# Kernel tuning notes

Measured on AMD Instinct MI355X. Metric: run time of the kernel, lower is better.

## Reference

```python
import jax, jax.numpy as jnp
import numpy as np

D_MODEL = 2048
NUM_HEADS = 16
D_K = D_MODEL // NUM_HEADS  # 128
THETA = 10000.0
BATCH = 2
SEQ = 2048


def _rope(v, pos):
    # v: [..., S, d_k], pos: [..., S] int
    half = v.shape[-1] // 2
    inv_freq = THETA ** (-(jnp.arange(half, dtype=jnp.float32) * 2.0) / v.shape[-1])
    ang = pos[..., None].astype(jnp.float32) * inv_freq  # [..., S, half]
    cos, sin = jnp.cos(ang), jnp.sin(ang)
    x1 = v[..., 0::2]
    x2 = v[..., 1::2]
    r1 = x1 * cos - x2 * sin
    r2 = x1 * sin + x2 * cos
    return jnp.stack([r1, r2], axis=-1).reshape(v.shape)


def setup_inputs() -> dict:
    key = jax.random.key(0)
    ks = jax.random.split(key, 5)
    scale = D_MODEL ** -0.5
    x = jax.random.normal(ks[0], (BATCH, SEQ, D_MODEL), dtype=jnp.float32)
    WQ = jax.random.normal(ks[1], (D_MODEL, D_MODEL), dtype=jnp.float32) * scale
    WK = jax.random.normal(ks[2], (D_MODEL, D_MODEL), dtype=jnp.float32) * scale
    WV = jax.random.normal(ks[3], (D_MODEL, D_MODEL), dtype=jnp.float32) * scale
    WO = jax.random.normal(ks[4], (D_MODEL, D_MODEL), dtype=jnp.float32) * scale
    token_positions = jnp.broadcast_to(jnp.arange(SEQ, dtype=jnp.int32), (BATCH, SEQ))
    return {"x": x, "token_positions": token_positions, "WQ": WQ, "WK": WK, "WV": WV, "WO": WO}


def reference(x, token_positions, WQ, WK, WV, WO):
    B, S, _ = x.shape
    split = lambda t: t.reshape(B, S, NUM_HEADS, D_K).transpose(0, 2, 1, 3)  # [B,H,S,d]
    Q = split(x @ WQ.T)
    K = split(x @ WK.T)
    V = split(x @ WV.T)
    pos = token_positions[:, None, :]  # broadcast over heads
    Q = _rope(Q, pos)
    K = _rope(K, pos)
    scores = jnp.einsum('bhqd,bhkd->bhqk', Q, K) / np.sqrt(D_K).astype(np.float32)
    causal = jnp.arange(S)[:, None] >= jnp.arange(S)[None, :]  # [S,S]
    scores = jnp.where(causal, scores, -jnp.inf)
    attn = jax.nn.softmax(scores, axis=-1)
    out = jnp.einsum('bhqk,bhkd->bhqd', attn, V)
    out = out.transpose(0, 2, 1, 3).reshape(B, S, D_MODEL)
    return out @ WO.T
```

## Files before the change

### kernel.cpp

```cpp
#include <hip/hip_runtime.h>

typedef unsigned short ushort;
typedef __attribute__((ext_vector_type(8))) __bf16 bf16x8;
typedef __attribute__((ext_vector_type(8))) ushort ushort8;
typedef __attribute__((ext_vector_type(4))) float f32x4;
typedef __attribute__((ext_vector_type(16))) float f32x16;
typedef __attribute__((ext_vector_type(4))) unsigned u32x4;

#define DM 2048
#define NH 16
#define DK 128
#define BATCH 2
#define SEQ 2048
#define MROWS (BATCH*SEQ)

#define GLDS16(g, l) __builtin_amdgcn_global_load_lds(                         \
    (const __attribute__((address_space(1))) void*)(g),                        \
    (__attribute__((address_space(3))) void*)(l), 16, 0, 0)

__device__ __forceinline__ ushort f2bf(float f) {
  unsigned u = __builtin_bit_cast(unsigned, f);
  u += 0x7fffu + ((u >> 16) & 1u);
  return (ushort)(u >> 16);
}

__device__ __forceinline__ unsigned cvtpk(float lo, float hi) {
  unsigned r;
  asm("v_cvt_pk_bf16_f32 %0, %1, %2" : "=v"(r) : "v"(lo), "v"(hi));
  return r;
}

__global__ __launch_bounds__(256) void cvt_all(const float* __restrict__ x,
                                               const float* __restrict__ w0,
                                               const float* __restrict__ w1,
                                               const float* __restrict__ w2,
                                               const float* __restrict__ w3,
                                               ushort* __restrict__ xb,
                                               ushort* __restrict__ o0,
                                               ushort* __restrict__ o1,
                                               ushort* __restrict__ o2,
                                               ushort* __restrict__ o3) {
  int b = blockIdx.x;
  const float* src;
  ushort* dst;
  int lb;
  if (b < 4096) { src = x; dst = xb; lb = b; }
  else {
    int wsel = (b - 4096) >> 11;
    lb = (b - 4096) & 2047;
    src = (wsel == 0) ? w0 : (wsel == 1) ? w1 : (wsel == 2) ? w2 : w3;
    dst = (wsel == 0) ? o0 : (wsel == 1) ? o1 : (wsel == 2) ? o2 : o3;
  }
  int i = lb * 256 + threadIdx.x;
  const float4* p = (const float4*)src;
  float4 a = p[2 * i], bq = p[2 * i + 1];
  ushort8 o;
  o[0] = f2bf(a.x); o[1] = f2bf(a.y); o[2] = f2bf(a.z); o[3] = f2bf(a.w);
  o[4] = f2bf(bq.x); o[5] = f2bf(bq.y); o[6] = f2bf(bq.z); o[7] = f2bf(bq.w);
  *(ushort8*)(dst + (size_t)8 * i) = o;
}

template <int NW, int NFR, int MODE>
__device__ __forceinline__ void gemmF_body(const ushort* __restrict__ A,
                                           const ushort* __restrict__ B0,
                                           const ushort* __restrict__ B1,
                                           const ushort* __restrict__ B2,
                                           ushort* __restrict__ O0,
                                           ushort* __restrict__ O1,
                                           ushort* __restrict__ O2,
                                           float* __restrict__ ofp,
                                           int row0, int col0) {
  extern __shared__ ushort lds[];
  constexpr int NT = DM / 64;
  constexpr int BUFSZ = 8192 + NW * NFR * 4096;
  const ushort* Bw[3] = {B0, B1, B2};
  ushort* Ow[3] = {O0, O1, O2};
  const int tid = threadIdx.x;
  const int wid = tid >> 6, lane = tid & 63;
  const int l15 = lane & 15, lhi = lane >> 4;
  const int wm = wid >> 2, wn = wid & 3;
  const int swz = l15 & 7;

  f32x4 acc[4][NW * NFR];
  const f32x4 z4 = {0.f, 0.f, 0.f, 0.f};
#pragma unroll
  for (int mq = 0; mq < 4; ++mq)
#pragma unroll
    for (int i = 0; i < NW * NFR; ++i) acc[mq][i] = z4;

  auto stage = [&](int kt, int buf) {
    ushort* dstA = &lds[buf * BUFSZ];
    const ushort* srcA = A + (size_t)row0 * DM + kt * 64;
#pragma unroll
    for (int j = 0; j < 2; ++j) {
      int g = j * 512 + tid;
      int r = g >> 3, c = g & 7;
      GLDS16(srcA + (size_t)r * DM + ((c ^ (r & 7)) * 8),
             &dstA[(j * 512 + wid * 64) * 8]);
    }
#pragma unroll
    for (int w3 = 0; w3 < NW; ++w3) {
      ushort* dstB = &lds[buf * BUFSZ + 8192 + w3 * NFR * 4096];
      const ushort* srcB = Bw[w3] + (size_t)col0 * DM + kt * 64;
#pragma unroll
      for (int j = 0; j < NFR; ++j) {
        int g = j * 512 + tid;
        int r = g >> 3, c = g & 7;
        GLDS16(srcB + (size_t)r * DM + ((c ^ (r & 7)) * 8),
               &dstB[(j * 512 + wid * 64) * 8]);
      }
    }
  };

  stage(0, 0);
  asm volatile("s_waitcnt vmcnt(0)" ::: "memory");
  asm volatile("s_barrier" ::: "memory");

  for (int t = 0; t < NT; ++t) {
    const int cb = t & 1;
    const ushort* Ab = &lds[cb * BUFSZ];
    const ushort* Bb = Ab + 8192;
    if (t + 1 < NT) stage(t + 1, cb ^ 1);
#pragma unroll
    for (int ks = 0; ks < 2; ++ks) {
      bf16x8 af[4];
#pragma unroll
      for (int mq = 0; mq < 4; ++mq) {
        int row = wm * 64 + mq * 16 + l15;
        af[mq] = *(const bf16x8*)&Ab[row * 64 + (((ks * 4 + lhi) ^ swz) * 8)];
      }
      bf16x8 bfr[NW * NFR];
#pragma unroll
      for (int w3 = 0; w3 < NW; ++w3)
#pragma unroll
        for (int n = 0; n < NFR; ++n) {
          int row = wn * (NFR * 16) + n * 16 + l15;
          bfr[w3 * NFR + n] =
              *(const bf16x8*)&Bb[w3 * NFR * 4096 + row * 64 + (((ks * 4 + lhi) ^ swz) * 8)];
        }
      __builtin_amdgcn_s_setprio(1);
#pragma unroll
      for (int mq = 0; mq < 4; ++mq)
#pragma unroll
        for (int i = 0; i < NW * NFR; ++i)
          acc[mq][i] = __builtin_amdgcn_mfma_f32_16x16x32_bf16(af[mq], bfr[i], acc[mq][i], 0, 0, 0);
      __builtin_amdgcn_s_setprio(0);
    }
    asm volatile("s_waitcnt vmcnt(0)" ::: "memory");
    asm volatile("s_barrier" ::: "memory");
  }

#pragma unroll
  for (int mq = 0; mq < 4; ++mq) {
    int grow = row0 + wm * 64 + mq * 16 + lhi * 4;
#pragma unroll
    for (int w3 = 0; w3 < NW; ++w3)
#pragma unroll
      for (int n = 0; n < NFR; ++n) {
        int gcol = col0 + wn * (NFR * 16) + n * 16 + l15;
#pragma unroll
        for (int j = 0; j < 4; ++j) {
          float v = acc[mq][w3 * NFR + n][j];
          int r = grow + j;
          if (MODE == 0) {
            int b = r >> 11, s = r & (SEQ - 1);
            int h = gcol >> 7, d = gcol & (DK - 1);
            Ow[w3][((size_t)(b * NH + h) * SEQ + s) * DK + d] = f2bf(v);
          } else {
            ofp[(size_t)r * DM + gcol] = v;
          }
        }
      }
  }
}

__global__ __launch_bounds__(512, 2) void gemmF_qkv(const ushort* __restrict__ A,
                                                    const ushort* __restrict__ W0,
                                                    const ushort* __restrict__ W1,
                                                    const ushort* __restrict__ W2,
                                                    ushort* __restrict__ O0,
                                                    ushort* __restrict__ O1,
                                                    ushort* __restrict__ O2) {
  int f = ((int)blockIdx.x & 7) * 64 + ((int)blockIdx.x >> 3);
  int row0 = (f >> 4) * 128, col0 = (f & 15) * 128;
  gemmF_body<3, 2, 0>(A, W0, W1, W2, O0, O1, O2, nullptr, row0, col0);
}

__global__ __launch_bounds__(512, 2) void gemmF_out(const ushort* __restrict__ A,
                                                    const ushort* __restrict__ Bm,
                                                    float* __restrict__ ofp) {
  int f = ((int)blockIdx.x & 7) * 32 + ((int)blockIdx.x >> 3);
  int row0 = (f >> 3) * 128, col0 = (f & 7) * 256;
  gemmF_body<1, 4, 1>(A, Bm, nullptr, nullptr, nullptr, nullptr, nullptr, ofp, row0, col0);
}

__global__ __launch_bounds__(256) void rope_kernel(ushort* __restrict__ Q,
                                                   ushort* __restrict__ K,
                                                   const int* __restrict__ tpos) {
  int bid = blockIdx.x;
  ushort* buf = (bid & 1) ? K : Q;
  int idx = (bid >> 1) * 256 + threadIdx.x;
  int c = idx & 15;
  int row = idx >> 4;
  int s = row & (SEQ - 1);
  int bh = row >> 11;
  int b = bh >> 4;
  int pos = tpos[b * SEQ + s];
  int d0 = c * 8;
  ushort8 v = *(ushort8*)(buf + (size_t)row * DK + d0);
  float fp = (float)pos;
#pragma unroll
  for (int p = 0; p < 4; ++p) {
    int i = (d0 >> 1) + p;
    float freq = exp2f(-13.287712379549449f * ((float)i * (1.0f / 64.0f)));
    float ang = fp * freq;
    float sn, cs;
    sincosf(ang, &sn, &cs);
    float x1 = __builtin_bit_cast(float, (unsigned)v[2 * p] << 16);
    float x2 = __builtin_bit_cast(float, (unsigned)v[2 * p + 1] << 16);
    float r1 = x1 * cs - x2 * sn;
    float r2 = x1 * sn + x2 * cs;
    v[2 * p] = f2bf(r1);
    v[2 * p + 1] = f2bf(r2);
  }
  *(ushort8*)(buf + (size_t)row * DK + d0) = v;
}

__global__ __launch_bounds__(256) void transpose_v(const ushort* __restrict__ Vb,
                                                   ushort* __restrict__ Vt) {
  __shared__ ushort t[64 * 80];
  int s0 = blockIdx.x * 64, d0 = blockIdx.y * 64, bh = blockIdx.z;
  const size_t base = (size_t)bh * SEQ * DK;
  int tid = threadIdx.x;
#pragma unroll
  for (int it = 0; it < 2; ++it) {
    int c = it * 256 + tid;
    int r = c >> 3, c8 = (c & 7) * 8;
    ushort8 v = *(const ushort8*)&Vb[base + (size_t)(s0 + r) * DK + d0 + c8];
    *(ushort8*)&t[r * 80 + c8] = v;
  }
  __syncthreads();
  const size_t obase = (size_t)bh * DK * SEQ;
#pragma unroll
  for (int it = 0; it < 2; ++it) {
    int c = it * 256 + tid;
    int dr = c >> 3, sc = (c & 7) * 8;
    ushort8 v;
#pragma unroll
    for (int i2 = 0; i2 < 8; ++i2) v[i2] = t[(sc + i2) * 80 + dr];
    *(ushort8*)&Vt[obase + (size_t)(d0 + dr) * SEQ + s0 + sc] = v;
  }
}

__global__ __launch_bounds__(256, 2) void attn_kernel(const ushort* __restrict__ Qb,
                                                      const ushort* __restrict__ Kb,
                                                      const ushort* __restrict__ Vt,
                                                      ushort* __restrict__ attnb) {
  __shared__ ushort lds[32768];
  const int bx = blockIdx.x;
  const int u = bx & 255, hg = bx >> 8;
  const int qt = hg ? (15 - (u & 15)) : (u & 15);
  const int bh = (u >> 4) + hg * 16;
  const int tid = threadIdx.x;
  const int w = tid >> 6, lane = tid & 63;
  const int l31 = lane & 31, hi = lane >> 5;
  const int qb = qt * 128;
  const int qsb = qb + w * 32;
  const int q = qsb + l31;
  const size_t qk_base = (size_t)bh * SEQ * DK;
  const size_t v_base = (size_t)bh * DK * SEQ;
  const int nt = (qb + 128) >> 6;

  bf16x8 qf[8];
#pragma unroll
  for (int ks = 0; ks < 8; ++ks)
    qf[ks] = *(const bf16x8*)&Qb[qk_base + (size_t)q * DK + ks * 16 + hi * 8];

  f32x16 acc[4];
#pragma unroll
  for (int dt = 0; dt < 4; ++dt)
#pragma unroll
    for (int r = 0; r < 16; ++r) acc[dt][r] = 0.f;

  float m2 = -INFINITY, lsum = 0.f;
  const float cs2 = 0.08838834764831845f * 1.4426950408889634f;

  auto stage = [&](int t, int bufsel) {
    const int kb0 = t * 64;
#pragma unroll
    for (int i = 0; i < 4; ++i) {
      int g = w * 256 + i * 64 + lane;
      int row = g >> 4, c16 = g & 15;
      GLDS16(Kb + qk_base + (size_t)(kb0 + row) * DK + ((c16 ^ (row & 7)) * 8),
             &lds[bufsel * 8192 + (w * 256 + i * 64) * 8]);
    }
#pragma unroll
    for (int i = 0; i < 4; ++i) {
      int g = w * 256 + i * 64 + lane;
      int row = g >> 3, c8 = g & 7;
      GLDS16(Vt + v_base + (size_t)row * SEQ + kb0 + ((c8 ^ (row & 7)) * 8),
             &lds[16384 + bufsel * 8192 + (w * 256 + i * 64) * 8]);
    }
  };

  stage(0, 0);
  __syncthreads();
  int buf = 0;

  for (int t = 0; t < nt; ++t) {
    if (t + 1 < nt) stage(t + 1, buf ^ 1);
    const int kb0 = t * 64;
    if (kb0 <= qsb) {
      const ushort* lk = &lds[buf * 8192];
      const ushort* lv = &lds[16384 + buf * 8192];
      const int kb1 = kb0 + 32;
      const bool diag0 = (kb0 == qsb);
      const bool have1 = (kb1 <= qsb);
      const bool diag1 = (kb1 == qsb);
      const int sw = l31 & 7;

      f32x16 s0, s1;
#pragma unroll
      for (int r = 0; r < 16; ++r) { s0[r] = 0.f; s1[r] = 0.f; }
      __builtin_amdgcn_s_setprio(1);
#pragma unroll
      for (int ks = 0; ks < 8; ++ks) {
        int g = 2 * ks + hi;
        bf16x8 kf = *(const bf16x8*)&lk[(l31 * 16 + (g ^ sw)) * 8];
        s0 = __builtin_amdgcn_mfma_f32_32x32x16_bf16(kf, qf[ks], s0, 0, 0, 0);
      }
      if (have1) {
#pragma unroll
        for (int ks = 0; ks < 8; ++ks) {
          int g = 2 * ks + hi;
          bf16x8 kf = *(const bf16x8*)&lk[((32 + l31) * 16 + (g ^ sw)) * 8];
          s1 = __builtin_amdgcn_mfma_f32_32x32x16_bf16(kf, qf[ks], s1, 0, 0, 0);
        }
      }
      __builtin_amdgcn_s_setprio(0);

      float mx = -INFINITY;
#pragma unroll
      for (int r = 0; r < 16; ++r) {
        float v = s0[r] * cs2;
        if (diag0) {
          int kk = kb0 + (r & 3) + 8 * (r >> 2) + 4 * hi;
          if (kk > q) v = -INFINITY;
        }
        s0[r] = v;
        mx = fmaxf(mx, v);
      }
      if (have1) {
#pragma unroll
        for (int r = 0; r < 16; ++r) {
          float v = s1[r] * cs2;
          if (diag1) {
            int kk = kb1 + (r & 3) + 8 * (r >> 2) + 4 * hi;
            if (kk > q) v = -INFINITY;
          }
          s1[r] = v;
          mx = fmaxf(mx, v);
        }
      }
      mx = fmaxf(mx, __shfl_xor(mx, 32));

      float sc = 1.f;
      if (!__all(mx <= m2 + 11.5f)) {
        float mnew = fmaxf(m2, mx);
        sc = exp2f(m2 - mnew);
        m2 = mnew;
#pragma unroll
        for (int dt = 0; dt < 4; ++dt)
#pragma unroll
          for (int r = 0; r < 16; ++r) acc[dt][r] *= sc;
      }
      float rs = 0.f;
#pragma unroll
      for (int r = 0; r < 16; ++r) {
        float p = exp2f(s0[r] - m2);
        s0[r] = p;
        rs += p;
      }
      if (have1) {
#pragma unroll
        for (int r = 0; r < 16; ++r) {
          float p = exp2f(s1[r] - m2);
          s1[r] = p;
          rs += p;
        }
      }
      rs += __shfl_xor(rs, 32);
      lsum = lsum * sc + rs;

      unsigned w0[8], ws0[8];
#pragma unroll
      for (int i = 0; i < 8; ++i) w0[i] = cvtpk(s0[2 * i], s0[2 * i + 1]);
#pragma unroll
      for (int i = 0; i < 8; ++i) ws0[i] = (unsigned)__shfl_xor((int)w0[i], 32);
      u32x4 b00, b01;
      b00[0] = hi ? ws0[2] : w0[0]; b00[1] = hi ? ws0[3] : w0[1];
      b00[2] = hi ? w0[2] : ws0[0]; b00[3] = hi ? w0[3] : ws0[1];
      b01[0] = hi ? ws0[6] : w0[4]; b01[1] = hi ? ws0[7] : w0[5];
      b01[2] = hi ? w0[6] : ws0[4]; b01[3] = hi ? w0[7] : ws0[5];
      bf16x8 pb00 = __builtin_bit_cast(bf16x8, b00);
      bf16x8 pb01 = __builtin_bit_cast(bf16x8, b01);
      bf16x8 pb10, pb11;
      if (have1) {
        unsigned w1[8], ws1[8];
#pragma unroll
        for (int i = 0; i < 8; ++i) w1[i] = cvtpk(s1[2 * i], s1[2 * i + 1]);
#pragma unroll
        for (int i = 0; i < 8; ++i) ws1[i] = (unsigned)__shfl_xor((int)w1[i], 32);
        u32x4 b10, b11;
        b10[0] = hi ? ws1[2] : w1[0]; b10[1] = hi ? ws1[3] : w1[1];
        b10[2] = hi ? w1[2] : ws1[0]; b10[3] = hi ? w1[3] : ws1[1];
        b11[0] = hi ? ws1[6] : w1[4]; b11[1] = hi ? ws1[7] : w1[5];
        b11[2] = hi ? w1[6] : ws1[4]; b11[3] = hi ? w1[7] : ws1[5];
        pb10 = __builtin_bit_cast(bf16x8, b10);
        pb11 = __builtin_bit_cast(bf16x8, b11);
      }

      __builtin_amdgcn_s_setprio(1);
#pragma unroll
      for (int dt = 0; dt < 4; ++dt) {
        int vr = (dt * 32 + l31) * 8;
        bf16x8 vf0 = *(const bf16x8*)&lv[(vr + ((0 + hi) ^ sw)) * 8];
        bf16x8 vf1 = *(const bf16x8*)&lv[(vr + ((2 + hi) ^ sw)) * 8];
        acc[dt] = __builtin_amdgcn_mfma_f32_32x32x16_bf16(vf0, pb00, acc[dt], 0, 0, 0);
        acc[dt] = __builtin_amdgcn_mfma_f32_32x32x16_bf16(vf1, pb01, acc[dt], 0, 0, 0);
        if (have1) {
          bf16x8 vf2 = *(const bf16x8*)&lv[(vr + ((4 + hi) ^ sw)) * 8];
          bf16x8 vf3 = *(const bf16x8*)&lv[(vr + ((6 + hi) ^ sw)) * 8];
          acc[dt] = __builtin_amdgcn_mfma_f32_32x32x16_bf16(vf2, pb10, acc[dt], 0, 0, 0);
          acc[dt] = __builtin_amdgcn_mfma_f32_32x32x16_bf16(vf3, pb11, acc[dt], 0, 0, 0);
        }
      }
      __builtin_amdgcn_s_setprio(0);
    }
    __syncthreads();
    buf ^= 1;
  }

  ushort* eo = &lds[w * 32 * 136];
  float inv = 1.0f / lsum;
#pragma unroll
  for (int dt = 0; dt < 4; ++dt)
#pragma unroll
    for (int rq = 0; rq < 4; ++rq) {
      unsigned lo = cvtpk(acc[dt][4 * rq] * inv, acc[dt][4 * rq + 1] * inv);
      unsigned hh = cvtpk(acc[dt][4 * rq + 2] * inv, acc[dt][4 * rq + 3] * inv);
      uint2 pr; pr.x = lo; pr.y = hh;
      *(uint2*)&eo[l31 * 136 + dt * 32 + rq * 8 + hi * 4] = pr;
    }
  const int b = bh >> 4, h = bh & (NH - 1);
#pragma unroll
  for (int it = 0; it < 8; ++it) {
    int row = it * 4 + (lane >> 4);
    int c8 = (lane & 15) * 8;
    ushort8 v = *(const ushort8*)&eo[row * 136 + c8];
    *(ushort8*)&attnb[((size_t)b * SEQ + qsb + row) * DM + h * DK + c8] = v;
  }
}

extern "C" void kernel_launch(void* const* d_in, const int* in_sizes, int n_in,
                              void* d_out, int out_size, void* d_ws, size_t ws_size,
                              hipStream_t stream) {
  const float* x = (const float*)d_in[0];
  const int* tpos = (const int*)d_in[1];
  const float* WQ = (const float*)d_in[2];
  const float* WK = (const float*)d_in[3];
  const float* WV = (const float*)d_in[4];
  const float* WO = (const float*)d_in[5];
  float* out = (float*)d_out;
  char* ws = (char*)d_ws;

  ushort* xb  = (ushort*)(ws + 0);
  ushort* wqb = (ushort*)(ws + 16777216);
  ushort* wkb = (ushort*)(ws + 25165824);
  ushort* wvb = (ushort*)(ws + 33554432);
  ushort* wob = (ushort*)(ws + 41943040);
  ushort* Qb  = (ushort*)(ws + 50331648);
  ushort* Kb  = (ushort*)(ws + 67108864);
  ushort* Vb  = (ushort*)(ws + 83886080);
  ushort* Vt  = (ushort*)(ws + 0);
  ushort* attnb = (ushort*)(ws + 16777216);

  hipFuncSetAttribute(reinterpret_cast<const void*>(gemmF_qkv),
                      hipFuncAttributeMaxDynamicSharedMemorySize, 131072);
  hipFuncSetAttribute(reinterpret_cast<const void*>(gemmF_out),
                      hipFuncAttributeMaxDynamicSharedMemorySize, 98304);

  cvt_all<<<12288, 256, 0, stream>>>(x, WQ, WK, WV, WO, xb, wqb, wkb, wvb, wob);

  gemmF_qkv<<<512, 512, 131072, stream>>>(xb, wqb, wkb, wvb, Qb, Kb, Vb);

  rope_kernel<<<8192, 256, 0, stream>>>(Qb, Kb, tpos);

  transpose_v<<<dim3(SEQ / 64, DK / 64, BATCH * NH), 256, 0, stream>>>(Vb, Vt);

  attn_kernel<<<dim3(512), 256, 0, stream>>>(Qb, Kb, Vt, attnb);

  gemmF_out<<<256, 512, 98304, stream>>>(attnb, wob, out);
}
```

Before: 257.7 us.

## Restructure GEMMs to K=32 tiles with two-stage prefetch and XCD-aware tiling

Both projection GEMMs now use 32-wide K tiles, which shrinks shared memory per block and lets the launch bound rise to four blocks per CU. The next tile is issued two iterations ahead and guarded by partial vmcnt waits, so loads overlap compute. The XOR swizzle is dropped, and the block-to-tile mapping groups tiles per XCD for L2 locality. The output GEMM switches to 128x128 tiles with twice as many blocks. Risks are LDS bank conflicts from the unswizzled 64-byte rows, twice as many barriers, and pressure to fit registers under the higher occupancy bound.

```diff
diff --git a/kernel.cpp b/kernel.cpp
--- a/kernel.cpp
+++ b/kernel.cpp
@@ -60,7 +60,7 @@
   *(ushort8*)(dst + (size_t)8 * i) = o;
 }
 
-template <int NW, int NFR, int MODE>
+template <int NW, int MODE>
 __device__ __forceinline__ void gemmF_body(const ushort* __restrict__ A,
                                            const ushort* __restrict__ B0,
                                            const ushort* __restrict__ B1,
@@ -71,83 +71,72 @@
                                            float* __restrict__ ofp,
                                            int row0, int col0) {
   extern __shared__ ushort lds[];
-  constexpr int NT = DM / 64;
-  constexpr int BUFSZ = 8192 + NW * NFR * 4096;
+  constexpr int NT = DM / 32;
+  constexpr int BUFSZ = 4096 * (1 + NW);
   const ushort* Bw[3] = {B0, B1, B2};
   ushort* Ow[3] = {O0, O1, O2};
   const int tid = threadIdx.x;
   const int wid = tid >> 6, lane = tid & 63;
   const int l15 = lane & 15, lhi = lane >> 4;
   const int wm = wid >> 2, wn = wid & 3;
-  const int swz = l15 & 7;
-
-  f32x4 acc[4][NW * NFR];
+
+  f32x4 acc[4][NW * 2];
   const f32x4 z4 = {0.f, 0.f, 0.f, 0.f};
 #pragma unroll
   for (int mq = 0; mq < 4; ++mq)
 #pragma unroll
-    for (int i = 0; i < NW * NFR; ++i) acc[mq][i] = z4;
-
+    for (int i = 0; i < NW * 2; ++i) acc[mq][i] = z4;
+
+  const int sr = tid >> 2, sc = tid & 3;
   auto stage = [&](int kt, int buf) {
-    ushort* dstA = &lds[buf * BUFSZ];
-    const ushort* srcA = A + (size_t)row0 * DM + kt * 64;
-#pragma unroll
-    for (int j = 0; j < 2; ++j) {
-      int g = j * 512 + tid;
-      int r = g >> 3, c = g & 7;
-      GLDS16(srcA + (size_t)r * DM + ((c ^ (r & 7)) * 8),
-             &dstA[(j * 512 + wid * 64) * 8]);
-    }
+    ushort* base = &lds[buf * BUFSZ];
+    const ushort* srcA = A + (size_t)row0 * DM + kt * 32;
+    GLDS16(srcA + (size_t)sr * DM + sc * 8, base + wid * 512);
 #pragma unroll
     for (int w3 = 0; w3 < NW; ++w3) {
-      ushort* dstB = &lds[buf * BUFSZ + 8192 + w3 * NFR * 4096];
-      const ushort* srcB = Bw[w3] + (size_t)col0 * DM + kt * 64;
-#pragma unroll
-      for (int j = 0; j < NFR; ++j) {
-        int g = j * 512 + tid;
-        int r = g >> 3, c = g & 7;
-        GLDS16(srcB + (size_t)r * DM + ((c ^ (r & 7)) * 8),
-               &dstB[(j * 512 + wid * 64) * 8]);
-      }
+      const ushort* srcB = Bw[w3] + (size_t)col0 * DM + kt * 32;
+      GLDS16(srcB + (size_t)sr * DM + sc * 8, base + 4096 + w3 * 4096 + wid * 512);
     }
   };
 
   stage(0, 0);
-  asm volatile("s_waitcnt vmcnt(0)" ::: "memory");
-  asm volatile("s_barrier" ::: "memory");
+  stage(1, 1);
 
   for (int t = 0; t < NT; ++t) {
-    const int cb = t & 1;
-    const ushort* Ab = &lds[cb * BUFSZ];
-    const ushort* Bb = Ab + 8192;
-    if (t + 1 < NT) stage(t + 1, cb ^ 1);
-#pragma unroll
-    for (int ks = 0; ks < 2; ++ks) {
-      bf16x8 af[4];
-#pragma unroll
-      for (int mq = 0; mq < 4; ++mq) {
-        int row = wm * 64 + mq * 16 + l15;
-        af[mq] = *(const bf16x8*)&Ab[row * 64 + (((ks * 4 + lhi) ^ swz) * 8)];
-      }
-      bf16x8 bfr[NW * NFR];
-#pragma unroll
-      for (int w3 = 0; w3 < NW; ++w3)
-#pragma unroll
-        for (int n = 0; n < NFR; ++n) {
-          int row = wn * (NFR * 16) + n * 16 + l15;
-          bfr[w3 * NFR + n] =
-              *(const bf16x8*)&Bb[w3 * NFR * 4096 + row * 64 + (((ks * 4 + lhi) ^ swz) * 8)];
-        }
+    if (t + 1 < NT) {
+      if constexpr (NW == 3)
+        asm volatile("s_waitcnt vmcnt(4)" ::: "memory");
+      else
+        asm volatile("s_waitcnt vmcnt(2)" ::: "memory");
+    } else {
+      asm volatile("s_waitcnt vmcnt(0)" ::: "memory");
+    }
+    __builtin_amdgcn_s_barrier();
+
+    const ushort* Ab = &lds[(t & 1) * BUFSZ];
+    bf16x8 af[4];
+#pragma unroll
+    for (int mq = 0; mq < 4; ++mq)
+      af[mq] = *(const bf16x8*)&Ab[(wm * 64 + mq * 16 + l15) * 32 + lhi * 8];
+#pragma unroll
+    for (int w3 = 0; w3 < NW; ++w3) {
+      const ushort* Bb = Ab + 4096 + w3 * 4096;
+      bf16x8 bfr[2];
+#pragma unroll
+      for (int n = 0; n < 2; ++n)
+        bfr[n] = *(const bf16x8*)&Bb[(wn * 32 + n * 16 + l15) * 32 + lhi * 8];
       __builtin_amdgcn_s_setprio(1);
 #pragma unroll
       for (int mq = 0; mq < 4; ++mq)
 #pragma unroll
-        for (int i = 0; i < NW * NFR; ++i)
-          acc[mq][i] = __builtin_amdgcn_mfma_f32_16x16x32_bf16(af[mq], bfr[i], acc[mq][i], 0, 0, 0);
+        for (int n = 0; n < 2; ++n)
+          acc[mq][w3 * 2 + n] = __builtin_amdgcn_mfma_f32_16x16x32_bf16(
+              af[mq], bfr[n], acc[mq][w3 * 2 + n], 0, 0, 0);
       __builtin_amdgcn_s_setprio(0);
     }
-    asm volatile("s_waitcnt vmcnt(0)" ::: "memory");
-    asm volatile("s_barrier" ::: "memory");
+
+    __builtin_amdgcn_s_barrier();
+    if (t + 2 < NT) stage(t + 2, t & 1);
   }
 
 #pragma unroll
@@ -156,11 +145,11 @@
 #pragma unroll
     for (int w3 = 0; w3 < NW; ++w3)
 #pragma unroll
-      for (int n = 0; n < NFR; ++n) {
-        int gcol = col0 + wn * (NFR * 16) + n * 16 + l15;
+      for (int n = 0; n < 2; ++n) {
+        int gcol = col0 + wn * 32 + n * 16 + l15;
 #pragma unroll
         for (int j = 0; j < 4; ++j) {
-          float v = acc[mq][w3 * NFR + n][j];
+          float v = acc[mq][w3 * 2 + n][j];
           int r = grow + j;
           if (MODE == 0) {
             int b = r >> 11, s = r & (SEQ - 1);
@@ -174,24 +163,26 @@
   }
 }
 
-__global__ __launch_bounds__(512, 2) void gemmF_qkv(const ushort* __restrict__ A,
+__global__ __launch_bounds__(512, 4) void gemmF_qkv(const ushort* __restrict__ A,
                                                     const ushort* __restrict__ W0,
                                                     const ushort* __restrict__ W1,
                                                     const ushort* __restrict__ W2,
                                                     ushort* __restrict__ O0,
                                                     ushort* __restrict__ O1,
                                                     ushort* __restrict__ O2) {
-  int f = ((int)blockIdx.x & 7) * 64 + ((int)blockIdx.x >> 3);
-  int row0 = (f >> 4) * 128, col0 = (f & 15) * 128;
-  gemmF_body<3, 2, 0>(A, W0, W1, W2, O0, O1, O2, nullptr, row0, col0);
-}
-
-__global__ __launch_bounds__(512, 2) void gemmF_out(const ushort* __restrict__ A,
+  int xcd = (int)blockIdx.x & 7, i = (int)blockIdx.x >> 3;
+  int row0 = (((xcd >> 2) << 4) + (i >> 2)) * 128;
+  int col0 = (((xcd & 3) << 2) + (i & 3)) * 128;
+  gemmF_body<3, 0>(A, W0, W1, W2, O0, O1, O2, nullptr, row0, col0);
+}
+
+__global__ __launch_bounds__(512, 4) void gemmF_out(const ushort* __restrict__ A,
                                                     const ushort* __restrict__ Bm,
                                                     float* __restrict__ ofp) {
-  int f = ((int)blockIdx.x & 7) * 32 + ((int)blockIdx.x >> 3);
-  int row0 = (f >> 3) * 128, col0 = (f & 7) * 256;
-  gemmF_body<1, 4, 1>(A, Bm, nullptr, nullptr, nullptr, nullptr, nullptr, ofp, row0, col0);
+  int xcd = (int)blockIdx.x & 7, i = (int)blockIdx.x >> 3;
+  int row0 = (((xcd >> 1) << 3) + (i >> 3)) * 128;
+  int col0 = (((xcd & 1) << 3) + (i & 7)) * 128;
+  gemmF_body<1, 1>(A, Bm, nullptr, nullptr, nullptr, nullptr, nullptr, ofp, row0, col0);
 }
 
 __global__ __launch_bounds__(256) void rope_kernel(ushort* __restrict__ Q,
@@ -486,13 +477,13 @@
   ushort* attnb = (ushort*)(ws + 16777216);
 
   hipFuncSetAttribute(reinterpret_cast<const void*>(gemmF_qkv),
-                      hipFuncAttributeMaxDynamicSharedMemorySize, 131072);
+                      hipFuncAttributeMaxDynamicSharedMemorySize, 65536);
   hipFuncSetAttribute(reinterpret_cast<const void*>(gemmF_out),
-                      hipFuncAttributeMaxDynamicSharedMemorySize, 98304);
+                      hipFuncAttributeMaxDynamicSharedMemorySize, 32768);
 
   cvt_all<<<12288, 256, 0, stream>>>(x, WQ, WK, WV, WO, xb, wqb, wkb, wvb, wob);
 
-  gemmF_qkv<<<512, 512, 131072, stream>>>(xb, wqb, wkb, wvb, Qb, Kb, Vb);
+  gemmF_qkv<<<512, 512, 65536, stream>>>(xb, wqb, wkb, wvb, Qb, Kb, Vb);
 
   rope_kernel<<<8192, 256, 0, stream>>>(Qb, Kb, tpos);
 
@@ -500,5 +491,5 @@
 
   attn_kernel<<<dim3(512), 256, 0, stream>>>(Qb, Kb, Vt, attnb);
 
-  gemmF_out<<<256, 512, 98304, stream>>>(attnb, wob, out);
-}
+  gemmF_out<<<512, 512, 32768, stream>>>(attnb, wob, out);
+}
```

Result: slower. 384.9 us (+49.3%).
